# Kernel tuning notes

Measured on AMD Instinct MI355X. Metric: run time of the kernel, lower is better.

Reference implementation:

```python
import jax, jax.numpy as jnp
import numpy as np

B, S, D = 4, 2048, 1024
NEG = 1e9


def setup_inputs() -> dict:
    key = jax.random.key(0)
    ks = jax.random.split(key, 4)
    scale = 1.0 / np.sqrt(D)  # glorot-ish init scale for stability
    x = jax.random.normal(ks[0], (B, S, D), dtype=jnp.float32)
    Wq = jax.random.normal(ks[1], (D, D), dtype=jnp.float32) * scale
    Wk = jax.random.normal(ks[2], (D, D), dtype=jnp.float32) * scale
    Wv = jax.random.normal(ks[3], (D, D), dtype=jnp.float32) * scale
    bq = jnp.zeros((D,), jnp.float32)
    bk = jnp.zeros((D,), jnp.float32)
    bv = jnp.zeros((D,), jnp.float32)
    return {"x": x, "Wq": Wq, "bq": bq, "Wk": Wk, "bk": bk, "Wv": Wv, "bv": bv}


def reference(x, Wq, bq, Wk, bk, Wv, bv):
    # Dense projections (single head, no 1/sqrt(d) scaling, matching source)
    q = x @ Wq + bq                      # [B,S,D]
    k = x @ Wk + bk                      # [B,S,D]
    v = x @ Wv + bv                      # [B,S,D]
    scores = jnp.einsum('bqd,bkd->bqk', q, k)   # [B,S,S]
    seq = scores.shape[-1]
    mask = jnp.tril(jnp.ones((seq, seq), scores.dtype))  # lower-triangular causal
    scores = scores * mask - NEG * (1.0 - mask)
    weights = jax.nn.softmax(scores, axis=-1)
    return jnp.einsum('bqk,bkd->bqd', weights, v)
```

## Files before the change

kernel.cpp:

```cpp
#include <hip/hip_runtime.h>

typedef float f32x4  __attribute__((ext_vector_type(4)));
typedef _Float16 f16x8  __attribute__((ext_vector_type(8)));
typedef _Float16 f16x4v __attribute__((ext_vector_type(4)));
typedef _Float16 f16x8v __attribute__((ext_vector_type(8)));

__device__ inline void load_lds16(const _Float16* g, _Float16* l) {
    __builtin_amdgcn_global_load_lds((const __attribute__((address_space(1))) void*)g,
                                     (__attribute__((address_space(3))) void*)l, 16, 0, 0);
}

__global__ __launch_bounds__(256)
void convert_h(const float* __restrict__ X, _Float16* __restrict__ H, long n4)
{
    long i = (long)blockIdx.x * 256 + threadIdx.x;
    if (i >= n4) return;
    f32x4 v = ((const f32x4*)X)[i];
    f16x4v h;
#pragma unroll
    for (int k = 0; k < 4; ++k) h[k] = (_Float16)v[k];
    ((f16x4v*)H)[i] = h;
}

__global__ __launch_bounds__(256)
void transpose_w3(const float* __restrict__ Wq, const float* __restrict__ Wk,
                  const float* __restrict__ Wv,
                  _Float16* __restrict__ W2, _Float16* __restrict__ Wvt, int D)
{
    const int z = blockIdx.z;
    const float* W = (z == 0) ? Wq : (z == 1) ? Wk : Wv;

    __shared__ float t[32][33];
    const int tid = threadIdx.x;
    const int bx = blockIdx.x * 32, by = blockIdx.y * 32;
    const int c = tid & 31, r0 = tid >> 5;
#pragma unroll
    for (int r = r0; r < 32; r += 8)
        t[r][c] = W[(long)(by + r) * D + bx + c];
    __syncthreads();
#pragma unroll
    for (int r = r0; r < 32; r += 8) {
        float v = t[c][r];
        _Float16 h = (_Float16)v;
        if (z < 2) {
            const long nrow = (long)z * D + bx + r;
            W2[nrow * 2 * D + by + c]     = h;
            W2[nrow * 2 * D + D + by + c] = (_Float16)(v - (float)h);
        } else {
            Wvt[(long)(bx + r) * D + by + c] = h;
        }
    }
}

#define STAGES_T(NTHR, NQ, gb, ld, base0, kbase, dst)                           \
    {                                                                           \
        _Pragma("unroll")                                                       \
        for (int q_ = 0; q_ < (NQ); ++q_) {                                     \
            const int p_ = q_ * (NTHR) + tid;                                   \
            const int rp_ = p_ >> 3;                                            \
            const int gl_ = (p_ & 7) ^ (rp_ & 7);                               \
            const int row_ = rp_ + ((gl_ >> 2) << 7);                           \
            load_lds16((gb) + (long)((base0) + row_) * (ld) + (kbase) +         \
                           ((gl_ & 3) << 3),                                    \
                       (dst) + p_ * 8);                                         \
        }                                                                       \
    }

__global__ __launch_bounds__(512)
void proj8(const _Float16* __restrict__ x_h, const _Float16* __restrict__ W2,
           const _Float16* __restrict__ Wvt,
           _Float16* __restrict__ Q_h, _Float16* __restrict__ Khl,
           _Float16* __restrict__ Vt,
           const float* __restrict__ bq, const float* __restrict__ bk,
           const float* __restrict__ bv)
{
    constexpr int D = 1024, SEQ = 2048;
    __shared__ __align__(16) _Float16 lds[65536];

    const int orig = blockIdx.x;
    const bool isV = orig >= 256;
    int ct, rt, ldb, NT2;
    const _Float16* Bb;
    if (!isV) {
        const int x = orig & 7, i = orig >> 3;
        rt = x * 4 + (i & 3);  ct = i >> 2;
        Bb = W2;  ldb = 2 * D; NT2 = 64;
    } else {
        const int o = orig - 256, x = o & 7, i = o >> 3;
        rt = x * 4 + (i & 3);  ct = i >> 2;
        Bb = Wvt; ldb = D;     NT2 = 32;
    }
    const int row0 = rt * 256, col0 = ct * 256;

    const int tid = threadIdx.x;
    const int wave = tid >> 6, lane = tid & 63, l16 = lane & 15, quad = lane >> 4;
    const int wmh = (wave >> 2) * 128;
    const int wn  = (wave & 3) * 64;
    const int ahalf = (wave >> 2) << 2;

    STAGES_T(512, 2, x_h, D, row0, 0,  lds);
    STAGES_T(512, 2, Bb, ldb, col0, 0, lds + 32768);
    STAGES_T(512, 2, x_h, D, row0, 32, lds + 8192);
    STAGES_T(512, 2, Bb, ldb, col0, 32, lds + 32768 + 8192);
    asm volatile("s_waitcnt vmcnt(4)" ::: "memory");
    __builtin_amdgcn_s_barrier();

    f32x4 acc[8][4] = {};

    for (int s = 0; s < NT2; ++s) {
        _Float16* Asl = lds + (s & 3) * 8192;
        _Float16* Bsl = lds + 32768 + (s & 3) * 8192;
        const bool pf = (s + 2 < NT2);
        const int kA2 = ((s + 2) * 32) & (D - 1);
        const int kB2 = (s + 2) * 32;

        f16x8 b[4], a0[4];
#pragma unroll
        for (int j = 0; j < 4; ++j) {
            const int nr = wn + j * 16 + l16;
            const int rpb = nr & 127;
            const int gpb = ((((nr >> 7) << 2) | quad) ^ (rpb & 7));
            b[j] = *(const f16x8*)&Bsl[rpb * 64 + gpb * 8];
        }
#pragma unroll
        for (int il = 0; il < 4; ++il) {
            const int rp = il * 16 + l16;
            const int gpa = ((ahalf | quad) ^ (rp & 7));
            a0[il] = *(const f16x8*)&Asl[rp * 64 + gpa * 8];
        }
        if (pf) STAGES_T(512, 2, x_h, D, row0, kA2, lds + ((s + 2) & 3) * 8192);
        __builtin_amdgcn_s_setprio(1);
#pragma unroll
        for (int il = 0; il < 4; ++il)
#pragma unroll
            for (int j = 0; j < 4; ++j)
                acc[il][j] = __builtin_amdgcn_mfma_f32_16x16x32_f16(
                    a0[il], b[j], acc[il][j], 0, 0, 0);
        __builtin_amdgcn_s_setprio(0);

        f16x8 a1[4];
#pragma unroll
        for (int il = 0; il < 4; ++il) {
            const int rp = (il + 4) * 16 + l16;
            const int gpa = ((ahalf | quad) ^ (rp & 7));
            a1[il] = *(const f16x8*)&Asl[rp * 64 + gpa * 8];
        }
        if (pf) STAGES_T(512, 2, Bb, ldb, col0, kB2, lds + 32768 + ((s + 2) & 3) * 8192);
        __builtin_amdgcn_s_setprio(1);
#pragma unroll
        for (int il = 0; il < 4; ++il)
#pragma unroll
            for (int j = 0; j < 4; ++j)
                acc[4 + il][j] = __builtin_amdgcn_mfma_f32_16x16x32_f16(
                    a1[il], b[j], acc[4 + il][j], 0, 0, 0);
        __builtin_amdgcn_s_setprio(0);

        if (pf)                asm volatile("s_waitcnt vmcnt(4)" ::: "memory");
        else if (s + 2 == NT2) asm volatile("s_waitcnt vmcnt(0)" ::: "memory");
        __builtin_amdgcn_s_barrier();
    }

    if (!isV) {
        const bool isQ = ct < 4;
        const float* bias = isQ ? bq : bk;
#pragma unroll
        for (int j = 0; j < 4; ++j) {
            const int colg = col0 + wn + j * 16 + l16;
            const int cc = isQ ? colg : colg - D;
            const float bval = bias[cc];
#pragma unroll
            for (int i = 0; i < 8; ++i) {
                const int rb = row0 + wmh + i * 16 + quad * 4;
#pragma unroll
                for (int r = 0; r < 4; ++r) {
                    const float v = acc[i][j][r] + bval;
                    const _Float16 h = (_Float16)v;
                    if (isQ) {
                        Q_h[(long)(rb + r) * D + cc] = h;
                    } else {
                        Khl[(long)(rb + r) * 2048 + cc] = h;
                        Khl[(long)(rb + r) * 2048 + 1024 + cc] = (_Float16)(v - (float)h);
                    }
                }
            }
        }
    } else {
        _Float16* sVt = lds;
#pragma unroll
        for (int j = 0; j < 4; ++j) {
            const int cl = wn + j * 16 + l16;
            const float bval = bv[col0 + cl];
#pragma unroll
            for (int i = 0; i < 8; ++i) {
                f16x4v pk;
#pragma unroll
                for (int r = 0; r < 4; ++r) pk[r] = (_Float16)(acc[i][j][r] + bval);
                const int rowb = wmh * 2 + i * 32 + quad * 8;
                const int sb = cl * 512 + (rowb ^ ((cl & 31) << 4));
                *(f16x4v*)((char*)sVt + sb) = pk;
            }
        }
        __syncthreads();
        const int bb = row0 >> 11;
        const int s0 = row0 & (SEQ - 1);
        for (int idx = tid; idx < 8192; idx += 512) {
            const int cl = idx >> 5, r8 = idx & 31;
            const int sb = cl * 512 + ((r8 * 16) ^ ((cl & 31) << 4));
            f16x8v v = *(const f16x8v*)&((char*)sVt)[sb];
            *(f16x8v*)&Vt[((long)bb * D + col0 + cl) * SEQ + s0 + r8 * 8] = v;
        }
    }
}

__global__ __launch_bounds__(512)
void gemm_sc(const _Float16* __restrict__ Q, const _Float16* __restrict__ Khl,
             float* __restrict__ Sc)
{
    constexpr int D = 1024, S = 2048;
    __shared__ __align__(16) _Float16 lds[65536];

    const int bz = blockIdx.y;
    const int t = blockIdx.x;
    int rt = (int)((sqrtf(8.0f * t + 1.0f) - 1.0f) * 0.5f);
    while (rt * (rt + 1) / 2 > t) --rt;
    while ((rt + 1) * (rt + 2) / 2 <= t) ++rt;
    const int ct = t - rt * (rt + 1) / 2;

    const _Float16* gA = Q + (long)bz * S * D;
    const _Float16* gB = Khl + (long)bz * S * 2048;
    const int row0 = rt * 256, col0 = ct * 256;
    constexpr int NT2 = 64;

    const int tid = threadIdx.x;
    const int wave = tid >> 6, lane = tid & 63, l16 = lane & 15, quad = lane >> 4;
    const int wmh = (wave >> 2) * 128;
    const int wn  = (wave & 3) * 64;
    const int ahalf = (wave >> 2) << 2;

    STAGES_T(512, 2, gA, D, row0, 0,  lds);
    STAGES_T(512, 2, gB, 2048, col0, 0, lds + 32768);
    STAGES_T(512, 2, gA, D, row0, 32, lds + 8192);
    STAGES_T(512, 2, gB, 2048, col0, 32, lds + 32768 + 8192);
    asm volatile("s_waitcnt vmcnt(4)" ::: "memory");
    __builtin_amdgcn_s_barrier();

    f32x4 acc[8][4] = {};

    for (int s = 0; s < NT2; ++s) {
        _Float16* Asl = lds + (s & 3) * 8192;
        _Float16* Bsl = lds + 32768 + (s & 3) * 8192;
        const bool pf = (s + 2 < NT2);
        const int kA2 = ((s + 2) * 32) & (D - 1);
        const int kB2 = (s + 2) * 32;

        f16x8 b[4], a0[4];
#pragma unroll
        for (int j = 0; j < 4; ++j) {
            const int nr = wn + j * 16 + l16;
            const int rpb = nr & 127;
            const int gpb = ((((nr >> 7) << 2) | quad) ^ (rpb & 7));
            b[j] = *(const f16x8*)&Bsl[rpb * 64 + gpb * 8];
        }
#pragma unroll
        for (int il = 0; il < 4; ++il) {
            const int rp = il * 16 + l16;
            const int gpa = ((ahalf | quad) ^ (rp & 7));
            a0[il] = *(const f16x8*)&Asl[rp * 64 + gpa * 8];
        }
        if (pf) STAGES_T(512, 2, gA, D, row0, kA2, lds + ((s + 2) & 3) * 8192);
        __builtin_amdgcn_s_setprio(1);
#pragma unroll
        for (int il = 0; il < 4; ++il)
#pragma unroll
            for (int j = 0; j < 4; ++j)
                acc[il][j] = __builtin_amdgcn_mfma_f32_16x16x32_f16(
                    a0[il], b[j], acc[il][j], 0, 0, 0);
        __builtin_amdgcn_s_setprio(0);

        f16x8 a1[4];
#pragma unroll
        for (int il = 0; il < 4; ++il) {
            const int rp = (il + 4) * 16 + l16;
            const int gpa = ((ahalf | quad) ^ (rp & 7));
            a1[il] = *(const f16x8*)&Asl[rp * 64 + gpa * 8];
        }
        if (pf) STAGES_T(512, 2, gB, 2048, col0, kB2, lds + 32768 + ((s + 2) & 3) * 8192);
        __builtin_amdgcn_s_setprio(1);
#pragma unroll
        for (int il = 0; il < 4; ++il)
#pragma unroll
            for (int j = 0; j < 4; ++j)
                acc[4 + il][j] = __builtin_amdgcn_mfma_f32_16x16x32_f16(
                    a1[il], b[j], acc[4 + il][j], 0, 0, 0);
        __builtin_amdgcn_s_setprio(0);

        if (pf)                asm volatile("s_waitcnt vmcnt(4)" ::: "memory");
        else if (s + 2 == NT2) asm volatile("s_waitcnt vmcnt(0)" ::: "memory");
        __builtin_amdgcn_s_barrier();
    }

    float* cf = Sc + (long)bz * S * S;
#pragma unroll
    for (int j = 0; j < 4; ++j) {
        const int col = col0 + wn + j * 16 + l16;
#pragma unroll
        for (int i = 0; i < 8; ++i) {
            const int rb = row0 + wmh + i * 16 + quad * 4;
#pragma unroll
            for (int r = 0; r < 4; ++r)
                cf[(long)(rb + r) * S + col] = acc[i][j][r];
        }
    }
}

__global__ __launch_bounds__(256)
void gemm_pv(const _Float16* __restrict__ P, const _Float16* __restrict__ Vt,
             float* __restrict__ Out)
{
    constexpr int D = 1024, S = 2048;
    __shared__ __align__(16) _Float16 lds[49152];

    const int rt = 7 - (int)blockIdx.x;
    const int ct = blockIdx.y;
    const int bz = blockIdx.z;
    const _Float16* gA = P + (long)bz * S * S;
    const _Float16* gB = Vt + (long)bz * D * S;
    const int row0 = rt * 256, col0 = ct * 128;
    const int NT2 = (rt + 1) * 8;

    const int tid = threadIdx.x;
    const int wave = tid >> 6, lane = tid & 63, l16 = lane & 15, quad = lane >> 4;
    const int wmh = (wave >> 1) * 128;
    const int wn  = (wave & 1) * 64;
    const int ahalf = (wave >> 1) << 2;

#define STAGEB_PV(kbase, dst)                                                   \
    {                                                                           \
        _Pragma("unroll")                                                       \
        for (int q_ = 0; q_ < 2; ++q_) {                                        \
            const int p_ = q_ * 256 + tid;                                      \
            const int rp_ = p_ >> 3;                                            \
            const int gl_ = (p_ & 7) ^ (rp_ & 7);                               \
            const int row_ = rp_ + ((gl_ >> 2) << 6);                           \
            load_lds16(gB + (long)(col0 + row_) * S + (kbase) +                 \
                           ((gl_ & 3) << 3),                                    \
                       (dst) + p_ * 8);                                         \
        }                                                                       \
    }

    STAGES_T(256, 4, gA, S, row0, 0,  lds);
    STAGEB_PV(0, lds + 32768);
    STAGES_T(256, 4, gA, S, row0, 32, lds + 8192);
    STAGEB_PV(32, lds + 32768 + 4096);
    asm volatile("s_waitcnt vmcnt(6)" ::: "memory");
    __builtin_amdgcn_s_barrier();

    f32x4 acc[8][4] = {};

    for (int s = 0; s < NT2; ++s) {
        _Float16* Asl = lds + (s & 3) * 8192;
        _Float16* Bsl = lds + 32768 + (s & 3) * 4096;
        const bool pf = (s + 2 < NT2);
        const int k2 = (s + 2) * 32;

        f16x8 b[4], a[8];
#pragma unroll
        for (int j = 0; j < 4; ++j) {
            const int nr = wn + j * 16 + l16;
            const int rpb = nr & 63;
            const int gpb = ((((nr >> 6) << 2) | quad) ^ (rpb & 7));
            b[j] = *(const f16x8*)&Bsl[rpb * 64 + gpb * 8];
        }
#pragma unroll
        for (int il = 0; il < 8; ++il) {
            const int rp = il * 16 + l16;
            const int gpa = ((ahalf | quad) ^ (rp & 7));
            a[il] = *(const f16x8*)&Asl[rp * 64 + gpa * 8];
        }
        if (pf) {
            STAGES_T(256, 4, gA, S, row0, k2, lds + ((s + 2) & 3) * 8192);
            STAGEB_PV(k2, lds + 32768 + ((s + 2) & 3) * 4096);
        }
        __builtin_amdgcn_s_setprio(1);
#pragma unroll
        for (int il = 0; il < 8; ++il)
#pragma unroll
            for (int j = 0; j < 4; ++j)
                acc[il][j] = __builtin_amdgcn_mfma_f32_16x16x32_f16(
                    a[il], b[j], acc[il][j], 0, 0, 0);
        __builtin_amdgcn_s_setprio(0);

        if (pf)                asm volatile("s_waitcnt vmcnt(6)" ::: "memory");
        else if (s + 2 == NT2) asm volatile("s_waitcnt vmcnt(0)" ::: "memory");
        __builtin_amdgcn_s_barrier();
    }

    float* cf = Out + (long)bz * S * D;
#pragma unroll
    for (int j = 0; j < 4; ++j) {
        const int col = col0 + wn + j * 16 + l16;
#pragma unroll
        for (int i = 0; i < 8; ++i) {
            const int rb = row0 + wmh + i * 16 + quad * 4;
#pragma unroll
            for (int r = 0; r < 4; ++r)
                cf[(long)(rb + r) * D + col] = acc[i][j][r];
        }
    }
#undef STAGEB_PV
}

__global__ __launch_bounds__(256)
void softmax_kernel(const float* __restrict__ Sc, _Float16* __restrict__ P, int seq)
{
    const int r = blockIdx.x, b = blockIdx.y;
    const float* row = Sc + ((long)b * seq + r) * seq;
    _Float16* prow = P + ((long)b * seq + r) * seq;
    const int tid = threadIdx.x;
    const int cmax = ((r >> 8) + 1) << 8;
    const int c0 = tid * 8;

    float v[8];
    f32x4 v0, v1;
    if (c0 <= r) {
        const f32x4* rp = (const f32x4*)row;
        v0 = rp[tid * 2];
        v1 = rp[tid * 2 + 1];
    } else {
        v0 = (f32x4)(-3.0e38f);
        v1 = (f32x4)(-3.0e38f);
    }
    float lmax = -3.0e38f;
#pragma unroll
    for (int k = 0; k < 4; ++k) {
        v[k]     = (c0 + k     <= r) ? v0[k] : -3.0e38f;
        v[k + 4] = (c0 + k + 4 <= r) ? v1[k] : -3.0e38f;
    }
#pragma unroll
    for (int k = 0; k < 8; ++k) lmax = fmaxf(lmax, v[k]);

    __shared__ float red[256];
    red[tid] = lmax; __syncthreads();
    for (int s = 128; s > 0; s >>= 1) {
        if (tid < s) red[tid] = fmaxf(red[tid], red[tid + s]);
        __syncthreads();
    }
    const float m = red[0];
    __syncthreads();

    float lsum = 0.0f;
#pragma unroll
    for (int k = 0; k < 8; ++k) {
        float e = (v[k] > -1.0e38f) ? __expf(v[k] - m) : 0.0f;
        v[k] = e;
        lsum += e;
    }
    red[tid] = lsum; __syncthreads();
    for (int s = 128; s > 0; s >>= 1) {
        if (tid < s) red[tid] += red[tid + s];
        __syncthreads();
    }
    const float inv = 1.0f / red[0];

    if (c0 < cmax) {
        f16x8v o;
#pragma unroll
        for (int k = 0; k < 8; ++k) o[k] = (_Float16)(v[k] * inv);
        ((f16x8v*)prow)[tid] = o;
    }
}

extern "C" void kernel_launch(void* const* d_in, const int* in_sizes, int n_in,
                              void* d_out, int out_size, void* d_ws, size_t ws_size,
                              hipStream_t stream)
{
    constexpr int B = 4, S = 2048, D = 1024;
    constexpr long MB = 1024 * 1024;
    const float* x  = (const float*)d_in[0];
    const float* Wq = (const float*)d_in[1];
    const float* bq = (const float*)d_in[2];
    const float* Wk = (const float*)d_in[3];
    const float* bk = (const float*)d_in[4];
    const float* Wv = (const float*)d_in[5];
    const float* bv = (const float*)d_in[6];
    float* out = (float*)d_out;

    char* ws = (char*)d_ws;
    _Float16* x_h   = (_Float16*)(ws + 0);
    _Float16* W2    = (_Float16*)(ws + 16 * MB);
    _Float16* Wvt_h = (_Float16*)(ws + 24 * MB);
    float*    Sc    = (float*)(ws + 0);
    _Float16* Q_h   = (_Float16*)(ws + 64 * MB);
    _Float16* Khl   = (_Float16*)(ws + 80 * MB);
    _Float16* Vt    = (_Float16*)(ws + 112 * MB);
    _Float16* P     = (_Float16*)(ws + 128 * MB);

    const int M = B * S;
    dim3 blk(256);

    convert_h<<<(M * D / 4 + 255) / 256, blk, 0, stream>>>(x, x_h, (long)M * D / 4);
    transpose_w3<<<dim3(D / 32, D / 32, 3), blk, 0, stream>>>(
        Wq, Wk, Wv, W2, Wvt_h, D);

    proj8<<<dim3(384), dim3(512), 0, stream>>>(
        x_h, W2, Wvt_h, Q_h, Khl, Vt, bq, bk, bv);

    gemm_sc<<<dim3(36, B), dim3(512), 0, stream>>>(Q_h, Khl, Sc);

    softmax_kernel<<<dim3(S, B), blk, 0, stream>>>(Sc, P, S);

    gemm_pv<<<dim3(8, 8, B), dim3(256), 0, stream>>>(P, Vt, out);
}
```

Baseline: 317.6 us.

## Restructure QK^T GEMM mainloop into 8-phase ping-pong schedule with K=64 half-tiles

Rewrites the gemm_sc main loop to stage 128-row by 64-wide K half-tiles, and splits each K=128 iteration into eight phases. Each phase interleaves one async global-to-LDS prefetch, a small set of LDS reads and a burst of MFMAs, with barriers and explicit waitcnt between phases. The aim is to spread memory issue evenly across the compute, overlapping loads with MFMA and raising MFMA density per barrier. The cost is many more barriers per iteration and tighter LDS buffer reuse, which can add synchronisation stalls or hazards. The STAGES_T and STAGEB_PV macros also switch to do-while(0) form.

New measurement: 318.8 us. About the same (+0.4%).

```diff
diff --git a/kernel.cpp b/kernel.cpp
--- a/kernel.cpp
+++ b/kernel.cpp
@@ -53,7 +53,7 @@
 }
 
 #define STAGES_T(NTHR, NQ, gb, ld, base0, kbase, dst)                           \
-    {                                                                           \
+    do {                                                                        \
         _Pragma("unroll")                                                       \
         for (int q_ = 0; q_ < (NQ); ++q_) {                                     \
             const int p_ = q_ * (NTHR) + tid;                                   \
@@ -64,7 +64,7 @@
                            ((gl_ & 3) << 3),                                    \
                        (dst) + p_ * 8);                                         \
         }                                                                       \
-    }
+    } while (0)
 
 __global__ __launch_bounds__(512)
 void proj8(const _Float16* __restrict__ x_h, const _Float16* __restrict__ W2,
@@ -212,11 +212,23 @@
     }
 }
 
+#define STAGEH64(gb, ld, grow0, kbase, dstofs)                                  \
+    do {                                                                        \
+        _Pragma("unroll")                                                       \
+        for (int q_ = 0; q_ < 2; ++q_) {                                        \
+            const int p_ = q_ * 512 + tid;                                      \
+            const int rp_ = p_ >> 3;                                            \
+            const int o_ = (p_ & 7) ^ (rp_ & 7);                                \
+            load_lds16((gb) + (long)((grow0) + rp_) * (ld) + (kbase) + o_ * 8,  \
+                       lds + (dstofs) + p_ * 8);                                \
+        }                                                                       \
+    } while (0)
+
 __global__ __launch_bounds__(512)
 void gemm_sc(const _Float16* __restrict__ Q, const _Float16* __restrict__ Khl,
              float* __restrict__ Sc)
 {
-    constexpr int D = 1024, S = 2048;
+    constexpr int D = 1024, S = 2048, NIT = 16;
     __shared__ __align__(16) _Float16 lds[65536];
 
     const int bz = blockIdx.y;
@@ -229,86 +241,103 @@
     const _Float16* gA = Q + (long)bz * S * D;
     const _Float16* gB = Khl + (long)bz * S * 2048;
     const int row0 = rt * 256, col0 = ct * 256;
-    constexpr int NT2 = 64;
 
     const int tid = threadIdx.x;
     const int wave = tid >> 6, lane = tid & 63, l16 = lane & 15, quad = lane >> 4;
     const int wmh = (wave >> 2) * 128;
     const int wn  = (wave & 3) * 64;
-    const int ahalf = (wave >> 2) << 2;
-
-    STAGES_T(512, 2, gA, D, row0, 0,  lds);
-    STAGES_T(512, 2, gB, 2048, col0, 0, lds + 32768);
-    STAGES_T(512, 2, gA, D, row0, 32, lds + 8192);
-    STAGES_T(512, 2, gB, 2048, col0, 32, lds + 32768 + 8192);
+    const int hA  = wmh >> 7;
+    const int hB  = wn >> 7;
+
+    STAGEH64(gB, 2048, col0,       0,  0 * 8192 + 32768);
+    STAGEH64(gB, 2048, col0 + 128, 0,  1 * 8192 + 32768);
+    STAGEH64(gA, D,    row0,       0,  0 * 8192);
+    STAGEH64(gA, D,    row0 + 128, 0,  1 * 8192);
+    STAGEH64(gB, 2048, col0,       64, 2 * 8192 + 32768);
+    STAGEH64(gB, 2048, col0 + 128, 64, 3 * 8192 + 32768);
     asm volatile("s_waitcnt vmcnt(4)" ::: "memory");
     __builtin_amdgcn_s_barrier();
 
     f32x4 acc[8][4] = {};
-
-    for (int s = 0; s < NT2; ++s) {
-        _Float16* Asl = lds + (s & 3) * 8192;
-        _Float16* Bsl = lds + 32768 + (s & 3) * 8192;
-        const bool pf = (s + 2 < NT2);
-        const int kA2 = ((s + 2) * 32) & (D - 1);
-        const int kB2 = (s + 2) * 32;
-
-        f16x8 b[4], a0[4];
-#pragma unroll
-        for (int j = 0; j < 4; ++j) {
-            const int nr = wn + j * 16 + l16;
-            const int rpb = nr & 127;
-            const int gpb = ((((nr >> 7) << 2) | quad) ^ (rpb & 7));
-            b[j] = *(const f16x8*)&Bsl[rpb * 64 + gpb * 8];
-        }
-#pragma unroll
-        for (int il = 0; il < 4; ++il) {
-            const int rp = il * 16 + l16;
-            const int gpa = ((ahalf | quad) ^ (rp & 7));
-            a0[il] = *(const f16x8*)&Asl[rp * 64 + gpa * 8];
-        }
-        if (pf) STAGES_T(512, 2, gA, D, row0, kA2, lds + ((s + 2) & 3) * 8192);
-        __builtin_amdgcn_s_setprio(1);
-#pragma unroll
-        for (int il = 0; il < 4; ++il)
-#pragma unroll
-            for (int j = 0; j < 4; ++j)
-                acc[il][j] = __builtin_amdgcn_mfma_f32_16x16x32_f16(
-                    a0[il], b[j], acc[il][j], 0, 0, 0);
-        __builtin_amdgcn_s_setprio(0);
-
-        f16x8 a1[4];
-#pragma unroll
-        for (int il = 0; il < 4; ++il) {
-            const int rp = (il + 4) * 16 + l16;
-            const int gpa = ((ahalf | quad) ^ (rp & 7));
-            a1[il] = *(const f16x8*)&Asl[rp * 64 + gpa * 8];
-        }
-        if (pf) STAGES_T(512, 2, gB, 2048, col0, kB2, lds + 32768 + ((s + 2) & 3) * 8192);
-        __builtin_amdgcn_s_setprio(1);
-#pragma unroll
-        for (int il = 0; il < 4; ++il)
-#pragma unroll
-            for (int j = 0; j < 4; ++j)
-                acc[4 + il][j] = __builtin_amdgcn_mfma_f32_16x16x32_f16(
-                    a1[il], b[j], acc[4 + il][j], 0, 0, 0);
-        __builtin_amdgcn_s_setprio(0);
-
-        if (pf)                asm volatile("s_waitcnt vmcnt(4)" ::: "memory");
-        else if (s + 2 == NT2) asm volatile("s_waitcnt vmcnt(0)" ::: "memory");
-        __builtin_amdgcn_s_barrier();
+    f16x8 b[4][2];
+
+    for (int j = 0; j < NIT; ++j) {
+        const bool pf = (j + 1 < NIT);
+        const int kAo = ((2 * j + 1) * 64) & (D - 1);
+        const int kAe = ((2 * j + 2) * 64) & (D - 1);
+        const int kBe = (2 * j + 2) * 64;
+        const int kBo = (2 * j + 3) * 64;
+
+#pragma unroll
+        for (int p = 0; p < 8; ++p) {
+            const int c = p >> 2;
+            const int q = p & 3;
+
+            if (q == 0) {
+                const _Float16* Bb_ = lds + 32768 + (c * 2 + hB) * 8192;
+#pragma unroll
+                for (int jj = 0; jj < 4; ++jj) {
+                    const int rB = (wn + jj * 16 + l16) & 127;
+#pragma unroll
+                    for (int kk = 0; kk < 2; ++kk)
+                        b[jj][kk] = *(const f16x8*)&Bb_[rB * 64 +
+                                        ((((kk << 2) | quad) ^ (rB & 7)) << 3)];
+                }
+            }
+            f16x8 a[2][2];
+            {
+                const _Float16* Ab_ = lds + (c * 2 + hA) * 8192;
+#pragma unroll
+                for (int il = 0; il < 2; ++il) {
+                    const int r = q * 32 + il * 16 + l16;
+#pragma unroll
+                    for (int kk = 0; kk < 2; ++kk)
+                        a[il][kk] = *(const f16x8*)&Ab_[r * 64 +
+                                        ((((kk << 2) | quad) ^ (r & 7)) << 3)];
+                }
+            }
+            if (p == 0)            { STAGEH64(gA, D,    row0,       kAo, 2 * 8192); }
+            else if (p == 1)       { STAGEH64(gA, D,    row0 + 128, kAo, 3 * 8192); }
+            else if (p == 2 && pf) { STAGEH64(gB, 2048, col0,       kBe, 0 * 8192 + 32768); }
+            else if (p == 3 && pf) { STAGEH64(gB, 2048, col0 + 128, kBe, 1 * 8192 + 32768); }
+            else if (p == 4 && pf) { STAGEH64(gA, D,    row0,       kAe, 0 * 8192); }
+            else if (p == 5 && pf) { STAGEH64(gA, D,    row0 + 128, kAe, 1 * 8192); }
+            else if (p == 6 && pf) { STAGEH64(gB, 2048, col0,       kBo, 2 * 8192 + 32768); }
+            else if (p == 7 && pf) { STAGEH64(gB, 2048, col0 + 128, kBo, 3 * 8192 + 32768); }
+
+            __builtin_amdgcn_s_barrier();
+            asm volatile("s_waitcnt lgkmcnt(0)" ::: "memory");
+            __builtin_amdgcn_sched_barrier(0);
+            __builtin_amdgcn_s_setprio(1);
+#pragma unroll
+            for (int il = 0; il < 2; ++il)
+#pragma unroll
+                for (int jj = 0; jj < 4; ++jj)
+#pragma unroll
+                    for (int kk = 0; kk < 2; ++kk)
+                        acc[q * 2 + il][jj] = __builtin_amdgcn_mfma_f32_16x16x32_f16(
+                            a[il][kk], b[jj][kk], acc[q * 2 + il][jj], 0, 0, 0);
+            __builtin_amdgcn_s_setprio(0);
+
+            if (p == 3) {
+                if (pf) { asm volatile("s_waitcnt vmcnt(4)" ::: "memory"); }
+                else    { asm volatile("s_waitcnt vmcnt(0)" ::: "memory"); }
+            }
+            if (p == 7 && pf) { asm volatile("s_waitcnt vmcnt(4)" ::: "memory"); }
+            __builtin_amdgcn_s_barrier();
+        }
     }
 
     float* cf = Sc + (long)bz * S * S;
 #pragma unroll
-    for (int j = 0; j < 4; ++j) {
-        const int col = col0 + wn + j * 16 + l16;
+    for (int jj = 0; jj < 4; ++jj) {
+        const int col = col0 + wn + jj * 16 + l16;
 #pragma unroll
         for (int i = 0; i < 8; ++i) {
             const int rb = row0 + wmh + i * 16 + quad * 4;
 #pragma unroll
             for (int r = 0; r < 4; ++r)
-                cf[(long)(rb + r) * S + col] = acc[i][j][r];
+                cf[(long)(rb + r) * S + col] = acc[i][jj][r];
         }
     }
 }
@@ -335,7 +364,7 @@
     const int ahalf = (wave >> 1) << 2;
 
 #define STAGEB_PV(kbase, dst)                                                   \
-    {                                                                           \
+    do {                                                                        \
         _Pragma("unroll")                                                       \
         for (int q_ = 0; q_ < 2; ++q_) {                                        \
             const int p_ = q_ * 256 + tid;                                      \
@@ -346,7 +375,7 @@
                            ((gl_ & 3) << 3),                                    \
                        (dst) + p_ * 8);                                         \
         }                                                                       \
-    }
+    } while (0)
 
     STAGES_T(256, 4, gA, S, row0, 0,  lds);
     STAGEB_PV(0, lds + 32768);
```

## Move V projection into score GEMM launch and use smaller double-buffered tiles

Applied to the files above, without the earlier changes.

The V projection is split out of the combined projection kernel and co-scheduled with the causal QK^T score GEMM in a new launch of 544 smaller 256x128 tiles, each a 256-thread block. The intent is to fill the GPU better, since the score GEMM previously had only 144 large blocks. LDS use drops from a four-stage to a two-stage buffer with a full vmcnt(0) wait every iteration. This allows more blocks per CU but gives up prefetch depth. gemm_pv gets the same two-stage, smaller-LDS treatment, and the workspace layout is reorganized.

After: 355.1 us. 11.8% more time.

```diff
diff --git a/kernel.cpp b/kernel.cpp
--- a/kernel.cpp
+++ b/kernel.cpp
@@ -53,7 +53,7 @@
 }
 
 #define STAGES_T(NTHR, NQ, gb, ld, base0, kbase, dst)                           \
-    {                                                                           \
+    do {                                                                        \
         _Pragma("unroll")                                                       \
         for (int q_ = 0; q_ < (NQ); ++q_) {                                     \
             const int p_ = q_ * (NTHR) + tid;                                   \
@@ -64,33 +64,35 @@
                            ((gl_ & 3) << 3),                                    \
                        (dst) + p_ * 8);                                         \
         }                                                                       \
-    }
+    } while (0)
+
+#define STAGEB128(gb, ld, base0, kbase, dst)                                    \
+    do {                                                                        \
+        _Pragma("unroll")                                                       \
+        for (int q_ = 0; q_ < 2; ++q_) {                                        \
+            const int p_ = q_ * 256 + tid;                                      \
+            const int rp_ = p_ >> 3;                                            \
+            const int gl_ = (p_ & 7) ^ (rp_ & 7);                               \
+            const int row_ = rp_ + ((gl_ >> 2) << 6);                           \
+            load_lds16((gb) + (long)((base0) + row_) * (ld) + (kbase) +         \
+                           ((gl_ & 3) << 3),                                    \
+                       (dst) + p_ * 8);                                         \
+        }                                                                       \
+    } while (0)
 
 __global__ __launch_bounds__(512)
-void proj8(const _Float16* __restrict__ x_h, const _Float16* __restrict__ W2,
-           const _Float16* __restrict__ Wvt,
-           _Float16* __restrict__ Q_h, _Float16* __restrict__ Khl,
-           _Float16* __restrict__ Vt,
-           const float* __restrict__ bq, const float* __restrict__ bk,
-           const float* __restrict__ bv)
-{
-    constexpr int D = 1024, SEQ = 2048;
+void projQK(const _Float16* __restrict__ x_h, const _Float16* __restrict__ W2,
+            _Float16* __restrict__ Q_h, _Float16* __restrict__ Khl,
+            const float* __restrict__ bq, const float* __restrict__ bk)
+{
+    constexpr int D = 1024;
     __shared__ __align__(16) _Float16 lds[65536];
 
     const int orig = blockIdx.x;
-    const bool isV = orig >= 256;
-    int ct, rt, ldb, NT2;
-    const _Float16* Bb;
-    if (!isV) {
-        const int x = orig & 7, i = orig >> 3;
-        rt = x * 4 + (i & 3);  ct = i >> 2;
-        Bb = W2;  ldb = 2 * D; NT2 = 64;
-    } else {
-        const int o = orig - 256, x = o & 7, i = o >> 3;
-        rt = x * 4 + (i & 3);  ct = i >> 2;
-        Bb = Wvt; ldb = D;     NT2 = 32;
-    }
+    const int x = orig & 7, i = orig >> 3;
+    const int rt = x * 4 + (i & 3), ct = i >> 2;
     const int row0 = rt * 256, col0 = ct * 256;
+    constexpr int NT2 = 64;
 
     const int tid = threadIdx.x;
     const int wave = tid >> 6, lane = tid & 63, l16 = lane & 15, quad = lane >> 4;
@@ -99,9 +101,9 @@
     const int ahalf = (wave >> 2) << 2;
 
     STAGES_T(512, 2, x_h, D, row0, 0,  lds);
-    STAGES_T(512, 2, Bb, ldb, col0, 0, lds + 32768);
+    STAGES_T(512, 2, W2, 2048, col0, 0, lds + 32768);
     STAGES_T(512, 2, x_h, D, row0, 32, lds + 8192);
-    STAGES_T(512, 2, Bb, ldb, col0, 32, lds + 32768 + 8192);
+    STAGES_T(512, 2, W2, 2048, col0, 32, lds + 32768 + 8192);
     asm volatile("s_waitcnt vmcnt(4)" ::: "memory");
     __builtin_amdgcn_s_barrier();
 
@@ -145,7 +147,7 @@
             const int gpa = ((ahalf | quad) ^ (rp & 7));
             a1[il] = *(const f16x8*)&Asl[rp * 64 + gpa * 8];
         }
-        if (pf) STAGES_T(512, 2, Bb, ldb, col0, kB2, lds + 32768 + ((s + 2) & 3) * 8192);
+        if (pf) STAGES_T(512, 2, W2, 2048, col0, kB2, lds + 32768 + ((s + 2) & 3) * 8192);
         __builtin_amdgcn_s_setprio(1);
 #pragma unroll
         for (int il = 0; il < 4; ++il)
@@ -160,155 +162,161 @@
         __builtin_amdgcn_s_barrier();
     }
 
+    const bool isQ = ct < 4;
+    const float* bias = isQ ? bq : bk;
+#pragma unroll
+    for (int j = 0; j < 4; ++j) {
+        const int colg = col0 + wn + j * 16 + l16;
+        const int cc = isQ ? colg : colg - D;
+        const float bval = bias[cc];
+#pragma unroll
+        for (int i = 0; i < 8; ++i) {
+            const int rb = row0 + wmh + i * 16 + quad * 4;
+#pragma unroll
+            for (int r = 0; r < 4; ++r) {
+                const float v = acc[i][j][r] + bval;
+                const _Float16 h = (_Float16)v;
+                if (isQ) {
+                    Q_h[(long)(rb + r) * D + cc] = h;
+                } else {
+                    Khl[(long)(rb + r) * 2048 + cc] = h;
+                    Khl[(long)(rb + r) * 2048 + 1024 + cc] = (_Float16)(v - (float)h);
+                }
+            }
+        }
+    }
+}
+
+__global__ __launch_bounds__(256)
+void sc_v(const _Float16* __restrict__ Q, const _Float16* __restrict__ Khl,
+          float* __restrict__ Sc,
+          const _Float16* __restrict__ x_h, const _Float16* __restrict__ Wvt,
+          _Float16* __restrict__ Vt, const float* __restrict__ bv)
+{
+    constexpr int D = 1024, S = 2048;
+    __shared__ __align__(16) _Float16 lds[24576];
+
+    const int bx = blockIdx.x;
+    const bool isV = bx >= 288;
+
+    const int tid = threadIdx.x;
+    const int wave = tid >> 6, lane = tid & 63, l16 = lane & 15, quad = lane >> 4;
+    const int wmh = (wave >> 1) * 128;
+    const int wn  = (wave & 1) * 64;
+    const int ahalf = (wave >> 1) << 2;
+
+    const _Float16 *gA, *gB;
+    int row0, col0, NT2, ldb, bz;
     if (!isV) {
-        const bool isQ = ct < 4;
-        const float* bias = isQ ? bq : bk;
+        bz = bx / 72;
+        const int t = bx % 72;
+        int rt = (int)sqrtf((float)t);
+        while (rt * (rt + 1) > t) --rt;
+        while ((rt + 1) * (rt + 2) <= t) ++rt;
+        const int ct = t - rt * (rt + 1);
+        row0 = rt * 256; col0 = ct * 128;
+        gA = Q + (long)bz * S * D;
+        gB = Khl + (long)bz * S * 2048;
+        NT2 = 64; ldb = 2048;
+    } else {
+        const int o = bx - 288;
+        const int rtg = o & 31, ctv = o >> 5;
+        row0 = rtg * 256; col0 = ctv * 128;
+        gA = x_h;  gB = Wvt;
+        NT2 = 32; ldb = D;
+        bz = 0;
+    }
+
+    STAGES_T(256, 4, gA, D, row0, 0, lds);
+    STAGEB128(gB, ldb, col0, 0, lds + 16384);
+    asm volatile("s_waitcnt vmcnt(0)" ::: "memory");
+    __builtin_amdgcn_s_barrier();
+
+    f32x4 acc[8][4] = {};
+
+    for (int s = 0; s < NT2; ++s) {
+        _Float16* Asl = lds + (s & 1) * 8192;
+        _Float16* Bsl = lds + 16384 + (s & 1) * 4096;
+        const bool pf = (s + 1 < NT2);
+        const int kA = ((s + 1) * 32) & (D - 1);
+        const int kB = (s + 1) * 32;
+
+        f16x8 b[4], a[8];
 #pragma unroll
         for (int j = 0; j < 4; ++j) {
-            const int colg = col0 + wn + j * 16 + l16;
-            const int cc = isQ ? colg : colg - D;
-            const float bval = bias[cc];
+            const int nr = wn + j * 16 + l16;
+            const int rpb = nr & 63;
+            const int gpb = ((((nr >> 6) << 2) | quad) ^ (rpb & 7));
+            b[j] = *(const f16x8*)&Bsl[rpb * 64 + gpb * 8];
+        }
+#pragma unroll
+        for (int il = 0; il < 8; ++il) {
+            const int rp = il * 16 + l16;
+            const int gpa = ((ahalf | quad) ^ (rp & 7));
+            a[il] = *(const f16x8*)&Asl[rp * 64 + gpa * 8];
+        }
+        if (pf) {
+            STAGES_T(256, 4, gA, D, row0, kA, lds + ((s + 1) & 1) * 8192);
+            STAGEB128(gB, ldb, col0, kB, lds + 16384 + ((s + 1) & 1) * 4096);
+        }
+        __builtin_amdgcn_s_setprio(1);
+#pragma unroll
+        for (int il = 0; il < 8; ++il)
+#pragma unroll
+            for (int j = 0; j < 4; ++j)
+                acc[il][j] = __builtin_amdgcn_mfma_f32_16x16x32_f16(
+                    a[il], b[j], acc[il][j], 0, 0, 0);
+        __builtin_amdgcn_s_setprio(0);
+
+        asm volatile("s_waitcnt vmcnt(0)" ::: "memory");
+        __builtin_amdgcn_s_barrier();
+    }
+
+    if (!isV) {
+        float* cf = Sc + (long)bz * S * S;
+#pragma unroll
+        for (int j = 0; j < 4; ++j) {
+            const int col = col0 + wn + j * 16 + l16;
 #pragma unroll
             for (int i = 0; i < 8; ++i) {
                 const int rb = row0 + wmh + i * 16 + quad * 4;
 #pragma unroll
-                for (int r = 0; r < 4; ++r) {
-                    const float v = acc[i][j][r] + bval;
-                    const _Float16 h = (_Float16)v;
-                    if (isQ) {
-                        Q_h[(long)(rb + r) * D + cc] = h;
-                    } else {
-                        Khl[(long)(rb + r) * 2048 + cc] = h;
-                        Khl[(long)(rb + r) * 2048 + 1024 + cc] = (_Float16)(v - (float)h);
+                for (int r = 0; r < 4; ++r)
+                    cf[(long)(rb + r) * S + col] = acc[i][j][r];
+            }
+        }
+    } else {
+        _Float16* sVt = lds;
+        const int bb = row0 >> 11;
+        const int s0 = row0 & (S - 1);
+#pragma unroll
+        for (int ch = 0; ch < 2; ++ch) {
+            if ((wave & 1) == ch) {
+#pragma unroll
+                for (int j = 0; j < 4; ++j) {
+                    const int cl2 = j * 16 + l16;
+                    const float bval = bv[col0 + ch * 64 + cl2];
+#pragma unroll
+                    for (int i = 0; i < 8; ++i) {
+                        f16x4v pk;
+#pragma unroll
+                        for (int r = 0; r < 4; ++r)
+                            pk[r] = (_Float16)(acc[i][j][r] + bval);
+                        const int rowb = wmh * 2 + i * 32 + quad * 8;
+                        const int sb = cl2 * 512 + (rowb ^ ((cl2 & 31) << 4));
+                        *(f16x4v*)((char*)sVt + sb) = pk;
                     }
                 }
             }
-        }
-    } else {
-        _Float16* sVt = lds;
-#pragma unroll
-        for (int j = 0; j < 4; ++j) {
-            const int cl = wn + j * 16 + l16;
-            const float bval = bv[col0 + cl];
-#pragma unroll
-            for (int i = 0; i < 8; ++i) {
-                f16x4v pk;
-#pragma unroll
-                for (int r = 0; r < 4; ++r) pk[r] = (_Float16)(acc[i][j][r] + bval);
-                const int rowb = wmh * 2 + i * 32 + quad * 8;
-                const int sb = cl * 512 + (rowb ^ ((cl & 31) << 4));
-                *(f16x4v*)((char*)sVt + sb) = pk;
+            __syncthreads();
+            for (int idx = tid; idx < 2048; idx += 256) {
+                const int cl2 = idx >> 5, r8 = idx & 31;
+                const int sb = cl2 * 512 + ((r8 * 16) ^ ((cl2 & 31) << 4));
+                f16x8v v = *(const f16x8v*)((char*)sVt + sb);
+                *(f16x8v*)&Vt[((long)bb * D + col0 + ch * 64 + cl2) * S +
+                              s0 + r8 * 8] = v;
             }
-        }
-        __syncthreads();
-        const int bb = row0 >> 11;
-        const int s0 = row0 & (SEQ - 1);
-        for (int idx = tid; idx < 8192; idx += 512) {
-            const int cl = idx >> 5, r8 = idx & 31;
-            const int sb = cl * 512 + ((r8 * 16) ^ ((cl & 31) << 4));
-            f16x8v v = *(const f16x8v*)&((char*)sVt)[sb];
-            *(f16x8v*)&Vt[((long)bb * D + col0 + cl) * SEQ + s0 + r8 * 8] = v;
-        }
-    }
-}
-
-__global__ __launch_bounds__(512)
-void gemm_sc(const _Float16* __restrict__ Q, const _Float16* __restrict__ Khl,
-             float* __restrict__ Sc)
-{
-    constexpr int D = 1024, S = 2048;
-    __shared__ __align__(16) _Float16 lds[65536];
-
-    const int bz = blockIdx.y;
-    const int t = blockIdx.x;
-    int rt = (int)((sqrtf(8.0f * t + 1.0f) - 1.0f) * 0.5f);
-    while (rt * (rt + 1) / 2 > t) --rt;
-    while ((rt + 1) * (rt + 2) / 2 <= t) ++rt;
-    const int ct = t - rt * (rt + 1) / 2;
-
-    const _Float16* gA = Q + (long)bz * S * D;
-    const _Float16* gB = Khl + (long)bz * S * 2048;
-    const int row0 = rt * 256, col0 = ct * 256;
-    constexpr int NT2 = 64;
-
-    const int tid = threadIdx.x;
-    const int wave = tid >> 6, lane = tid & 63, l16 = lane & 15, quad = lane >> 4;
-    const int wmh = (wave >> 2) * 128;
-    const int wn  = (wave & 3) * 64;
-    const int ahalf = (wave >> 2) << 2;
-
-    STAGES_T(512, 2, gA, D, row0, 0,  lds);
-    STAGES_T(512, 2, gB, 2048, col0, 0, lds + 32768);
-    STAGES_T(512, 2, gA, D, row0, 32, lds + 8192);
-    STAGES_T(512, 2, gB, 2048, col0, 32, lds + 32768 + 8192);
-    asm volatile("s_waitcnt vmcnt(4)" ::: "memory");
-    __builtin_amdgcn_s_barrier();
-
-    f32x4 acc[8][4] = {};
-
-    for (int s = 0; s < NT2; ++s) {
-        _Float16* Asl = lds + (s & 3) * 8192;
-        _Float16* Bsl = lds + 32768 + (s & 3) * 8192;
-        const bool pf = (s + 2 < NT2);
-        const int kA2 = ((s + 2) * 32) & (D - 1);
-        const int kB2 = (s + 2) * 32;
-
-        f16x8 b[4], a0[4];
-#pragma unroll
-        for (int j = 0; j < 4; ++j) {
-            const int nr = wn + j * 16 + l16;
-            const int rpb = nr & 127;
-            const int gpb = ((((nr >> 7) << 2) | quad) ^ (rpb & 7));
-            b[j] = *(const f16x8*)&Bsl[rpb * 64 + gpb * 8];
-        }
-#pragma unroll
-        for (int il = 0; il < 4; ++il) {
-            const int rp = il * 16 + l16;
-            const int gpa = ((ahalf | quad) ^ (rp & 7));
-            a0[il] = *(const f16x8*)&Asl[rp * 64 + gpa * 8];
-        }
-        if (pf) STAGES_T(512, 2, gA, D, row0, kA2, lds + ((s + 2) & 3) * 8192);
-        __builtin_amdgcn_s_setprio(1);
-#pragma unroll
-        for (int il = 0; il < 4; ++il)
-#pragma unroll
-            for (int j = 0; j < 4; ++j)
-                acc[il][j] = __builtin_amdgcn_mfma_f32_16x16x32_f16(
-                    a0[il], b[j], acc[il][j], 0, 0, 0);
-        __builtin_amdgcn_s_setprio(0);
-
-        f16x8 a1[4];
-#pragma unroll
-        for (int il = 0; il < 4; ++il) {
-            const int rp = (il + 4) * 16 + l16;
-            const int gpa = ((ahalf | quad) ^ (rp & 7));
-            a1[il] = *(const f16x8*)&Asl[rp * 64 + gpa * 8];
-        }
-        if (pf) STAGES_T(512, 2, gB, 2048, col0, kB2, lds + 32768 + ((s + 2) & 3) * 8192);
-        __builtin_amdgcn_s_setprio(1);
-#pragma unroll
-        for (int il = 0; il < 4; ++il)
-#pragma unroll
-            for (int j = 0; j < 4; ++j)
-                acc[4 + il][j] = __builtin_amdgcn_mfma_f32_16x16x32_f16(
-                    a1[il], b[j], acc[4 + il][j], 0, 0, 0);
-        __builtin_amdgcn_s_setprio(0);
-
-        if (pf)                asm volatile("s_waitcnt vmcnt(4)" ::: "memory");
-        else if (s + 2 == NT2) asm volatile("s_waitcnt vmcnt(0)" ::: "memory");
-        __builtin_amdgcn_s_barrier();
-    }
-
-    float* cf = Sc + (long)bz * S * S;
-#pragma unroll
-    for (int j = 0; j < 4; ++j) {
-        const int col = col0 + wn + j * 16 + l16;
-#pragma unroll
-        for (int i = 0; i < 8; ++i) {
-            const int rb = row0 + wmh + i * 16 + quad * 4;
-#pragma unroll
-            for (int r = 0; r < 4; ++r)
-                cf[(long)(rb + r) * S + col] = acc[i][j][r];
+            __syncthreads();
         }
     }
 }
@@ -318,7 +326,7 @@
              float* __restrict__ Out)
 {
     constexpr int D = 1024, S = 2048;
-    __shared__ __align__(16) _Float16 lds[49152];
+    __shared__ __align__(16) _Float16 lds[24576];
 
     const int rt = 7 - (int)blockIdx.x;
     const int ct = blockIdx.y;
@@ -334,34 +342,18 @@
     const int wn  = (wave & 1) * 64;
     const int ahalf = (wave >> 1) << 2;
 
-#define STAGEB_PV(kbase, dst)                                                   \
-    {                                                                           \
-        _Pragma("unroll")                                                       \
-        for (int q_ = 0; q_ < 2; ++q_) {                                        \
-            const int p_ = q_ * 256 + tid;                                      \
-            const int rp_ = p_ >> 3;                                            \
-            const int gl_ = (p_ & 7) ^ (rp_ & 7);                               \
-            const int row_ = rp_ + ((gl_ >> 2) << 6);                           \
-            load_lds16(gB + (long)(col0 + row_) * S + (kbase) +                 \
-                           ((gl_ & 3) << 3),                                    \
-                       (dst) + p_ * 8);                                         \
-        }                                                                       \
-    }
-
-    STAGES_T(256, 4, gA, S, row0, 0,  lds);
-    STAGEB_PV(0, lds + 32768);
-    STAGES_T(256, 4, gA, S, row0, 32, lds + 8192);
-    STAGEB_PV(32, lds + 32768 + 4096);
-    asm volatile("s_waitcnt vmcnt(6)" ::: "memory");
+    STAGES_T(256, 4, gA, S, row0, 0, lds);
+    STAGEB128(gB, S, col0, 0, lds + 16384);
+    asm volatile("s_waitcnt vmcnt(0)" ::: "memory");
     __builtin_amdgcn_s_barrier();
 
     f32x4 acc[8][4] = {};
 
     for (int s = 0; s < NT2; ++s) {
-        _Float16* Asl = lds + (s & 3) * 8192;
-        _Float16* Bsl = lds + 32768 + (s & 3) * 4096;
-        const bool pf = (s + 2 < NT2);
-        const int k2 = (s + 2) * 32;
+        _Float16* Asl = lds + (s & 1) * 8192;
+        _Float16* Bsl = lds + 16384 + (s & 1) * 4096;
+        const bool pf = (s + 1 < NT2);
+        const int k1 = (s + 1) * 32;
 
         f16x8 b[4], a[8];
 #pragma unroll
@@ -378,8 +370,8 @@
             a[il] = *(const f16x8*)&Asl[rp * 64 + gpa * 8];
         }
         if (pf) {
-            STAGES_T(256, 4, gA, S, row0, k2, lds + ((s + 2) & 3) * 8192);
-            STAGEB_PV(k2, lds + 32768 + ((s + 2) & 3) * 4096);
+            STAGES_T(256, 4, gA, S, row0, k1, lds + ((s + 1) & 1) * 8192);
+            STAGEB128(gB, S, col0, k1, lds + 16384 + ((s + 1) & 1) * 4096);
         }
         __builtin_amdgcn_s_setprio(1);
 #pragma unroll
@@ -390,8 +382,7 @@
                     a[il], b[j], acc[il][j], 0, 0, 0);
         __builtin_amdgcn_s_setprio(0);
 
-        if (pf)                asm volatile("s_waitcnt vmcnt(6)" ::: "memory");
-        else if (s + 2 == NT2) asm volatile("s_waitcnt vmcnt(0)" ::: "memory");
+        asm volatile("s_waitcnt vmcnt(0)" ::: "memory");
         __builtin_amdgcn_s_barrier();
     }
 
@@ -407,7 +398,6 @@
                 cf[(long)(rb + r) * D + col] = acc[i][j][r];
         }
     }
-#undef STAGEB_PV
 }
 
 __global__ __launch_bounds__(256)
@@ -486,28 +476,22 @@
     float* out = (float*)d_out;
 
     char* ws = (char*)d_ws;
-    _Float16* x_h   = (_Float16*)(ws + 0);
-    _Float16* W2    = (_Float16*)(ws + 16 * MB);
-    _Float16* Wvt_h = (_Float16*)(ws + 24 * MB);
-    float*    Sc    = (float*)(ws + 0);
-    _Float16* Q_h   = (_Float16*)(ws + 64 * MB);
-    _Float16* Khl   = (_Float16*)(ws + 80 * MB);
-    _Float16* Vt    = (_Float16*)(ws + 112 * MB);
-    _Float16* P     = (_Float16*)(ws + 128 * MB);
+    _Float16* x_h = (_Float16*)(ws + 0);
+    _Float16* Wvt = (_Float16*)(ws + 16 * MB);
+    _Float16* Q_h = (_Float16*)(ws + 18 * MB);
+    _Float16* Khl = (_Float16*)(ws + 34 * MB);
+    _Float16* Vt  = (_Float16*)(ws + 66 * MB);
+    float*    Sc  = (float*)(ws + 82 * MB);
+    _Float16* W2  = (_Float16*)(ws + 146 * MB);
+    _Float16* P   = (_Float16*)(ws + 0);
 
     const int M = B * S;
     dim3 blk(256);
 
     convert_h<<<(M * D / 4 + 255) / 256, blk, 0, stream>>>(x, x_h, (long)M * D / 4);
-    transpose_w3<<<dim3(D / 32, D / 32, 3), blk, 0, stream>>>(
-        Wq, Wk, Wv, W2, Wvt_h, D);
-
-    proj8<<<dim3(384), dim3(512), 0, stream>>>(
-        x_h, W2, Wvt_h, Q_h, Khl, Vt, bq, bk, bv);
-
-    gemm_sc<<<dim3(36, B), dim3(512), 0, stream>>>(Q_h, Khl, Sc);
-
+    transpose_w3<<<dim3(D / 32, D / 32, 3), blk, 0, stream>>>(Wq, Wk, Wv, W2, Wvt, D);
+    projQK<<<dim3(256), dim3(512), 0, stream>>>(x_h, W2, Q_h, Khl, bq, bk);
+    sc_v<<<dim3(544), blk, 0, stream>>>(Q_h, Khl, Sc, x_h, Wvt, Vt, bv);
     softmax_kernel<<<dim3(S, B), blk, 0, stream>>>(Sc, P, S);
-
-    gemm_pv<<<dim3(8, 8, B), dim3(256), 0, stream>>>(P, Vt, out);
-}
+    gemm_pv<<<dim3(8, 8, B), blk, 0, stream>>>(P, Vt, out);
+}
```
